# Optimization experiments

Hardware: AMD Instinct MI355X
Metric: run time of the kernel (lower is better)

Reference implementation:

```python
import jax, jax.numpy as jnp
import numpy as np

B, L, S, H = 2, 256, 384, 768
Tc, Dc = 16, 50
WV, WD = 20000, 100
CV = 128
NEG = -1e30


def _lstm_scan(x, Wih, Whh, bih, bhh):
    # x: [N, T, D] -> hs: [N, T, Hc]; torch LSTM gate order i,f,g,o
    N = x.shape[0]
    Hc = Whh.shape[1]
    h0 = jnp.zeros((N, Hc), x.dtype)

    def step(carry, xt):
        h, c = carry
        g = xt @ Wih.T + h @ Whh.T + bih + bhh  # [N, 4Hc]
        i, f, gg, o = jnp.split(g, 4, axis=-1)
        i = jax.nn.sigmoid(i)
        f = jax.nn.sigmoid(f)
        gg = jnp.tanh(gg)
        o = jax.nn.sigmoid(o)
        c = f * c + i * gg
        h = o * jnp.tanh(c)
        return (h, c), h

    _, hs = jax.lax.scan(step, (h0, h0), jnp.swapaxes(x, 0, 1))
    return jnp.swapaxes(hs, 0, 1)


def setup_inputs() -> dict:
    key = jax.random.key(0)
    ks = jax.random.split(key, 10)
    bert_emb = jax.random.normal(ks[0], (B, S, H), jnp.float32)
    pieces2word = jax.random.randint(ks[1], (B, L, S), 0, 2, jnp.int32)
    word_ids = jax.random.randint(ks[2], (B, L), 0, WV, jnp.int32)
    char_count = jax.random.randint(ks[3], (B, L), 1, Tc + 1, jnp.int32)
    char_ids = jax.random.randint(ks[4], (B, L, Tc), 0, CV, jnp.int32)
    # mask consistent with ragged char lengths (first char_count positions valid)
    token_masks_char = (jnp.arange(Tc)[None, None, :] < char_count[..., None]).astype(jnp.int32)
    word_table = jax.random.normal(ks[5], (WV, WD), jnp.float32) * 0.02
    char_table = jax.random.normal(ks[6], (CV, Dc), jnp.float32) * 0.02
    sc = 1.0 / np.sqrt(Dc)

    def lstm_w(k):
        a, b, c, d = jax.random.split(k, 4)
        return (jax.random.uniform(a, (4 * Dc, Dc), jnp.float32, -sc, sc),
                jax.random.uniform(b, (4 * Dc, Dc), jnp.float32, -sc, sc),
                jax.random.uniform(c, (4 * Dc,), jnp.float32, -sc, sc),
                jax.random.uniform(d, (4 * Dc,), jnp.float32, -sc, sc))

    Wih_f, Whh_f, bih_f, bhh_f = lstm_w(ks[7])
    Wih_b, Whh_b, bih_b, bhh_b = lstm_w(ks[8])
    return dict(bert_emb=bert_emb, pieces2word=pieces2word, word_ids=word_ids,
                char_count=char_count, char_ids=char_ids, token_masks_char=token_masks_char,
                word_table=word_table, char_table=char_table,
                Wih_f=Wih_f, Whh_f=Whh_f, bih_f=bih_f, bhh_f=bhh_f,
                Wih_b=Wih_b, Whh_b=Whh_b, bih_b=bih_b, bhh_b=bhh_b)


def reference(bert_emb, pieces2word, word_ids, char_count, char_ids, token_masks_char,
              word_table, char_table, Wih_f, Whh_f, bih_f, bhh_f, Wih_b, Whh_b, bih_b, bhh_b):
    # --- piece2word max pool (expand + masked_fill(min) + max over pieces) ---
    minv = jnp.min(bert_emb)
    # [B, L, S, H] intermediate, as in the original expand
    masked = jnp.where(pieces2word[..., None] != 0, bert_emb[:, None, :, :], minv)
    word_reps = jnp.max(masked, axis=2)  # [B, L, H]
    # dropouts are identity in eval mode

    # --- word embedding lookup ---
    word_embed = word_table[word_ids]  # [B, L, WD]

    # --- char bi-LSTM with packed-sequence semantics ---
    lens = jnp.maximum(char_count.reshape(-1), 1)  # char_count[char_count==0]=1
    x = char_table[char_ids.reshape(B * L, Tc)]  # [N, Tc, Dc]
    h_fwd = _lstm_scan(x, Wih_f, Whh_f, bih_f, bhh_f)
    # reverse each sequence within its valid length for the backward direction
    t = jnp.arange(Tc)[None, :]
    idx = jnp.where(t < lens[:, None], lens[:, None] - 1 - t, t)  # [N, Tc]
    x_rev = jnp.take_along_axis(x, idx[..., None], axis=1)
    h_bwd = _lstm_scan(x_rev, Wih_b, Whh_b, bih_b, bhh_b)
    h_bwd = jnp.take_along_axis(h_bwd, idx[..., None], axis=1)  # back to original order
    h = jnp.concatenate([h_fwd, h_bwd], axis=-1)  # [N, Tc, 2*Dc]
    valid = (t < lens[:, None])[..., None]
    h = jnp.where(valid, h, 0.0)  # pad_packed_sequence zero-pads beyond length
    h = h.reshape(B, L, Tc, 2 * Dc)

    # --- combine(..., 'max'): masked max over ragged char groups ---
    m = jnp.where(token_masks_char[..., None] == 0, NEG, 0.0)
    sup = jnp.max(m + h, axis=2)  # [B, L, 2*Dc]
    sup = jnp.where(sup == NEG, 0.0, sup)

    return jnp.concatenate([word_reps, word_embed, sup], axis=-1)  # [B, L, H+WD+2*Dc]
```

## Files before the change

### kernel.cpp

```cpp
#include <hip/hip_runtime.h>
#include <float.h>

#define Bb 2
#define Ll 256
#define Ss 384
#define Hh 768
#define Tc 16
#define Dc 50
#define WD 100
#define OUTC 968


__global__ void init_ws(unsigned* wmin) {
    if (blockIdx.x == 0 && threadIdx.x == 0) *wmin = 0xFFFFFFFFu;
}

__device__ inline unsigned enc_f32(float f) {
    unsigned k = __float_as_uint(f);
    return (k & 0x80000000u) ? ~k : (k | 0x80000000u);
}
__device__ inline float dec_f32(unsigned k) {
    unsigned bits = (k & 0x80000000u) ? (k ^ 0x80000000u) : ~k;
    return __uint_as_float(bits);
}

__global__ void min_reduce(const float* __restrict__ x, int n, unsigned* wmin) {
    int i = blockIdx.x * blockDim.x + threadIdx.x;
    float m = FLT_MAX;
    for (; i < n; i += gridDim.x * blockDim.x) m = fminf(m, x[i]);
    #pragma unroll
    for (int off = 32; off; off >>= 1) m = fminf(m, __shfl_down(m, off, 64));
    if ((threadIdx.x & 63) == 0) atomicMin(wmin, enc_f32(m));
}


#define NCHUNK 4
#define SCHUNK (Ss / NCHUNK)
#define LT 8

__global__ __launch_bounds__(256) void word_reps_partial(
        const float* __restrict__ bert, const int* __restrict__ p2w,
        float* __restrict__ partial) {
    int blk = blockIdx.x;
    int hc = blk % 3;
    int lt = (blk / 3) % 32;
    int bc = blk / (3 * 32);
    int b  = bc >> 2;
    int ch = bc & 3;
    int h  = hc * 256 + threadIdx.x;
    int l0 = lt * LT;

    float acc[LT];
    #pragma unroll
    for (int i = 0; i < LT; i++) acc[i] = -FLT_MAX;

    const float* bb = bert + ((size_t)b * Ss) * Hh + h;
    const int*   pm = p2w + ((size_t)b * Ll + l0) * Ss;
    int s0 = ch * SCHUNK;
    for (int s = s0; s < s0 + SCHUNK; s++) {
        float v = bb[(size_t)s * Hh];
        #pragma unroll
        for (int i = 0; i < LT; i++) {
            int m = pm[i * Ss + s];
            acc[i] = fmaxf(acc[i], m ? v : -FLT_MAX);
        }
    }
    #pragma unroll
    for (int i = 0; i < LT; i++)
        partial[(((size_t)ch * Bb + b) * Ll + (l0 + i)) * Hh + h] = acc[i];
}


__device__ inline float tanh_fast(float x) {
    float e = __expf(2.f * x);
    return 1.f - 2.f / (e + 1.f);
}
__device__ inline float sigmoid_fast(float x) {
    return 1.f / (1.f + __expf(-x));
}

__global__ __launch_bounds__(256) void lstm_kernel(
        const int* __restrict__ char_ids, const int* __restrict__ char_count,
        const float* __restrict__ char_table,
        const float* __restrict__ Wih_f, const float* __restrict__ Whh_f,
        const float* __restrict__ bih_f, const float* __restrict__ bhh_f,
        const float* __restrict__ Wih_b, const float* __restrict__ Whh_b,
        const float* __restrict__ bih_b, const float* __restrict__ bhh_b,
        float* __restrict__ out) {
    int n   = blockIdx.x;
    int dir = blockIdx.y;
    const float* Wih = dir ? Wih_b : Wih_f;
    const float* Whh = dir ? Whh_b : Whh_f;
    const float* bih = dir ? bih_b : bih_f;
    const float* bhh = dir ? bhh_b : bhh_f;
    int tid = threadIdx.x;

    __shared__ __align__(16) float xs[Tc][52];
    __shared__ float xp[Tc][200];
    __shared__ float gs[200];
    __shared__ __align__(16) float hs[52];

    int len = char_count[n];
    if (len < 1) len = 1;

    for (int e = tid; e < Tc * 52; e += 256) {
        int t = e / 52, d = e - t * 52;
        int st = dir ? (t < len ? len - 1 - t : t) : t;
        float v = 0.f;
        if (d < Dc) v = char_table[char_ids[n * Tc + st] * Dc + d];
        xs[t][d] = v;
    }
    if (tid < 52) hs[tid] = 0.f;
    __syncthreads();

    float w[52];
    float bias = 0.f;
    if (tid < 200) {
        #pragma unroll
        for (int j = 0; j < Dc; j++) w[j] = Wih[tid * Dc + j];
        w[50] = 0.f; w[51] = 0.f;
        bias = bih[tid] + bhh[tid];
        for (int t = 0; t < Tc; t++) {
            float a = bias;
            #pragma unroll
            for (int j = 0; j < 52; j += 4) {
                float4 xv = *(const float4*)&xs[t][j];
                a += xv.x * w[j] + xv.y * w[j+1] + xv.z * w[j+2] + xv.w * w[j+3];
            }
            xp[t][tid] = a;
        }
        #pragma unroll
        for (int j = 0; j < Dc; j++) w[j] = Whh[tid * Dc + j];
    }
    __syncthreads();

    float c = 0.f, maxv = -FLT_MAX;
    for (int t = 0; t < Tc; t++) {
        if (tid < 200) {
            float g = xp[t][tid];
            #pragma unroll
            for (int j = 0; j < 52; j += 4) {
                float4 hv = *(const float4*)&hs[j];
                g += hv.x * w[j] + hv.y * w[j+1] + hv.z * w[j+2] + hv.w * w[j+3];
            }
            gs[tid] = g;
        }
        __syncthreads();
        if (tid < Dc) {
            float si = sigmoid_fast(gs[tid]);
            float sf = sigmoid_fast(gs[tid + 50]);
            float tg = tanh_fast(gs[tid + 100]);
            float so = sigmoid_fast(gs[tid + 150]);
            c = sf * c + si * tg;
            float h = so * tanh_fast(c);
            hs[tid] = h;
            if (t < len) maxv = fmaxf(maxv, h);
        }
        __syncthreads();
    }
    if (tid < Dc)
        out[(size_t)n * OUTC + (Hh + WD) + dir * Dc + tid] = maxv;
}


__global__ __launch_bounds__(256) void finalize(
        const float* __restrict__ partial, const unsigned* __restrict__ wmin,
        const int* __restrict__ word_ids, const float* __restrict__ word_table,
        float* __restrict__ out) {
    int idx = blockIdx.x * blockDim.x + threadIdx.x;
    if (idx >= Bb * Ll * OUTC) return;
    int col = idx % OUTC;
    int bl  = idx / OUTC;
    if (col < Hh) {
        float m = -FLT_MAX;
        #pragma unroll
        for (int ch = 0; ch < NCHUNK; ch++)
            m = fmaxf(m, partial[((size_t)ch * Bb * Ll + bl) * Hh + col]);
        if (m == -FLT_MAX) m = dec_f32(*wmin);
        out[idx] = m;
    } else if (col < Hh + WD) {
        out[idx] = word_table[(size_t)word_ids[bl] * WD + (col - Hh)];
    }
}

extern "C" void kernel_launch(void* const* d_in, const int* in_sizes, int n_in,
                              void* d_out, int out_size, void* d_ws, size_t ws_size,
                              hipStream_t stream) {
    const float* bert       = (const float*)d_in[0];
    const int*   p2w        = (const int*)d_in[1];
    const int*   word_ids   = (const int*)d_in[2];
    const int*   char_count = (const int*)d_in[3];
    const int*   char_ids   = (const int*)d_in[4];
    const float* word_table = (const float*)d_in[6];
    const float* char_table = (const float*)d_in[7];
    const float* Wih_f = (const float*)d_in[8];
    const float* Whh_f = (const float*)d_in[9];
    const float* bih_f = (const float*)d_in[10];
    const float* bhh_f = (const float*)d_in[11];
    const float* Wih_b = (const float*)d_in[12];
    const float* Whh_b = (const float*)d_in[13];
    const float* bih_b = (const float*)d_in[14];
    const float* bhh_b = (const float*)d_in[15];
    float* out = (float*)d_out;

    unsigned* wmin  = (unsigned*)d_ws;
    float* partial  = (float*)((char*)d_ws + 256);

    init_ws<<<1, 64, 0, stream>>>(wmin);
    min_reduce<<<256, 256, 0, stream>>>(bert, Bb * Ss * Hh, wmin);
    word_reps_partial<<<768, 256, 0, stream>>>(bert, p2w, partial);
    lstm_kernel<<<dim3(512, 2), 256, 0, stream>>>(
        char_ids, char_count, char_table,
        Wih_f, Whh_f, bih_f, bhh_f, Wih_b, Whh_b, bih_b, bhh_b, out);
    finalize<<<(Bb * Ll * OUTC + 255) / 256, 256, 0, stream>>>(
        partial, wmin, word_ids, word_table, out);
}
```

Before: 153.9 us.

## Precompute char input projections, fuse prep work, and write word reps directly

The input-to-hidden LSTM projection is precomputed once per vocabulary character (128 chars x 2 directions) into a table, so the per-word LSTM blocks only gather their gate pre-activations. The min reduction, the projection table and the word-embedding gather are merged into a single prep kernel. The word max-pool now runs over the full sequence per block with 4 rows per block and writes straight to the output, which removes the partial buffer, the atomics and the finalize pass. The cost is fewer, longer-running word blocks and a dependency on the prep kernel.

```diff
diff --git a/kernel.cpp b/kernel.cpp
--- a/kernel.cpp
+++ b/kernel.cpp
@@ -8,67 +8,9 @@
 #define Tc 16
 #define Dc 50
 #define WD 100
+#define CV 128
+#define NG 200
 #define OUTC 968
-
-
-__global__ void init_ws(unsigned* wmin) {
-    if (blockIdx.x == 0 && threadIdx.x == 0) *wmin = 0xFFFFFFFFu;
-}
-
-__device__ inline unsigned enc_f32(float f) {
-    unsigned k = __float_as_uint(f);
-    return (k & 0x80000000u) ? ~k : (k | 0x80000000u);
-}
-__device__ inline float dec_f32(unsigned k) {
-    unsigned bits = (k & 0x80000000u) ? (k ^ 0x80000000u) : ~k;
-    return __uint_as_float(bits);
-}
-
-__global__ void min_reduce(const float* __restrict__ x, int n, unsigned* wmin) {
-    int i = blockIdx.x * blockDim.x + threadIdx.x;
-    float m = FLT_MAX;
-    for (; i < n; i += gridDim.x * blockDim.x) m = fminf(m, x[i]);
-    #pragma unroll
-    for (int off = 32; off; off >>= 1) m = fminf(m, __shfl_down(m, off, 64));
-    if ((threadIdx.x & 63) == 0) atomicMin(wmin, enc_f32(m));
-}
-
-
-#define NCHUNK 4
-#define SCHUNK (Ss / NCHUNK)
-#define LT 8
-
-__global__ __launch_bounds__(256) void word_reps_partial(
-        const float* __restrict__ bert, const int* __restrict__ p2w,
-        float* __restrict__ partial) {
-    int blk = blockIdx.x;
-    int hc = blk % 3;
-    int lt = (blk / 3) % 32;
-    int bc = blk / (3 * 32);
-    int b  = bc >> 2;
-    int ch = bc & 3;
-    int h  = hc * 256 + threadIdx.x;
-    int l0 = lt * LT;
-
-    float acc[LT];
-    #pragma unroll
-    for (int i = 0; i < LT; i++) acc[i] = -FLT_MAX;
-
-    const float* bb = bert + ((size_t)b * Ss) * Hh + h;
-    const int*   pm = p2w + ((size_t)b * Ll + l0) * Ss;
-    int s0 = ch * SCHUNK;
-    for (int s = s0; s < s0 + SCHUNK; s++) {
-        float v = bb[(size_t)s * Hh];
-        #pragma unroll
-        for (int i = 0; i < LT; i++) {
-            int m = pm[i * Ss + s];
-            acc[i] = fmaxf(acc[i], m ? v : -FLT_MAX);
-        }
-    }
-    #pragma unroll
-    for (int i = 0; i < LT; i++)
-        partial[(((size_t)ch * Bb + b) * Ll + (l0 + i)) * Hh + h] = acc[i];
-}
 
 
 __device__ inline float tanh_fast(float x) {
@@ -79,65 +21,129 @@
     return 1.f / (1.f + __expf(-x));
 }
 
+
+__global__ __launch_bounds__(256) void prep_kernel(
+        const float* __restrict__ bert, const float* __restrict__ char_table,
+        const float* __restrict__ Wih_f, const float* __restrict__ bih_f, const float* __restrict__ bhh_f,
+        const float* __restrict__ Wih_b, const float* __restrict__ bih_b, const float* __restrict__ bhh_b,
+        const int* __restrict__ word_ids, const float* __restrict__ word_table,
+        float* __restrict__ minp, float* __restrict__ xpt, float* __restrict__ out) {
+    int blk = blockIdx.x, tid = threadIdx.x;
+    if (blk < 256) {
+        const int n = Bb * Ss * Hh;
+        float m = FLT_MAX;
+        for (int i = blk * 256 + tid; i < n; i += 256 * 256) m = fminf(m, bert[i]);
+        #pragma unroll
+        for (int off = 32; off; off >>= 1) m = fminf(m, __shfl_down(m, off, 64));
+        __shared__ float red[4];
+        if ((tid & 63) == 0) red[tid >> 6] = m;
+        __syncthreads();
+        if (tid == 0) minp[blk] = fminf(fminf(red[0], red[1]), fminf(red[2], red[3]));
+    } else if (blk < 512) {
+        int idx = blk - 256;
+        int dir = idx >> 7, cid = idx & 127;
+        const float* Wih = dir ? Wih_b : Wih_f;
+        const float* bih = dir ? bih_b : bih_f;
+        const float* bhh = dir ? bhh_b : bhh_f;
+        __shared__ float ct[Dc];
+        if (tid < Dc) ct[tid] = char_table[cid * Dc + tid];
+        __syncthreads();
+        if (tid < NG) {
+            float a = bih[tid] + bhh[tid];
+            #pragma unroll
+            for (int j = 0; j < Dc; j++) a += Wih[tid * Dc + j] * ct[j];
+            xpt[idx * NG + tid] = a;
+        }
+    } else {
+        for (int i = (blk - 512) * 256 + tid; i < Bb * Ll * WD; i += 64 * 256) {
+            int bl = i / WD, d = i - bl * WD;
+            out[(size_t)bl * OUTC + Hh + d] = word_table[(size_t)word_ids[bl] * WD + d];
+        }
+    }
+}
+
+
+__global__ __launch_bounds__(256) void word_kernel(
+        const float* __restrict__ bert, const int* __restrict__ p2w,
+        const float* __restrict__ minp, float* __restrict__ out) {
+    int tid = threadIdx.x;
+    __shared__ float sminv;
+    if (tid < 64) {
+        float m = fminf(fminf(minp[tid], minp[tid + 64]),
+                        fminf(minp[tid + 128], minp[tid + 192]));
+        #pragma unroll
+        for (int off = 32; off; off >>= 1) m = fminf(m, __shfl_down(m, off, 64));
+        if (tid == 0) sminv = m;
+    }
+    __syncthreads();
+    int blk = blockIdx.x;
+    int hc = blk % 3;
+    int lt = (blk / 3) & 63;
+    int b  = blk / 192;
+    int h  = hc * 256 + tid;
+    int l0 = lt * 4;
+
+    float acc[4];
+    #pragma unroll
+    for (int i = 0; i < 4; i++) acc[i] = -FLT_MAX;
+
+    const float* bb = bert + (size_t)b * Ss * Hh + h;
+    const int*   pm = p2w + ((size_t)b * Ll + l0) * Ss;
+    for (int s = 0; s < Ss; s++) {
+        float v = bb[(size_t)s * Hh];
+        #pragma unroll
+        for (int i = 0; i < 4; i++) {
+            int m = pm[i * Ss + s];
+            acc[i] = fmaxf(acc[i], m ? v : -FLT_MAX);
+        }
+    }
+    float mv = sminv;
+    #pragma unroll
+    for (int i = 0; i < 4; i++) {
+        float a = (acc[i] == -FLT_MAX) ? mv : acc[i];
+        out[((size_t)(b * Ll + l0 + i)) * OUTC + h] = a;
+    }
+}
+
+
 __global__ __launch_bounds__(256) void lstm_kernel(
         const int* __restrict__ char_ids, const int* __restrict__ char_count,
-        const float* __restrict__ char_table,
-        const float* __restrict__ Wih_f, const float* __restrict__ Whh_f,
-        const float* __restrict__ bih_f, const float* __restrict__ bhh_f,
-        const float* __restrict__ Wih_b, const float* __restrict__ Whh_b,
-        const float* __restrict__ bih_b, const float* __restrict__ bhh_b,
-        float* __restrict__ out) {
-    int n   = blockIdx.x;
-    int dir = blockIdx.y;
-    const float* Wih = dir ? Wih_b : Wih_f;
+        const float* __restrict__ Whh_f, const float* __restrict__ Whh_b,
+        const float* __restrict__ xpt, float* __restrict__ out) {
+    int n = blockIdx.x, dir = blockIdx.y, tid = threadIdx.x;
     const float* Whh = dir ? Whh_b : Whh_f;
-    const float* bih = dir ? bih_b : bih_f;
-    const float* bhh = dir ? bhh_b : bhh_f;
-    int tid = threadIdx.x;
-
-    __shared__ __align__(16) float xs[Tc][52];
-    __shared__ float xp[Tc][200];
-    __shared__ float gs[200];
+
+    __shared__ float xg[Tc][NG];
+    __shared__ float gs[NG];
     __shared__ __align__(16) float hs[52];
+    __shared__ int scid[Tc];
 
     int len = char_count[n];
     if (len < 1) len = 1;
-
-    for (int e = tid; e < Tc * 52; e += 256) {
-        int t = e / 52, d = e - t * 52;
+    if (tid < Tc) {
+        int t = tid;
         int st = dir ? (t < len ? len - 1 - t : t) : t;
-        float v = 0.f;
-        if (d < Dc) v = char_table[char_ids[n * Tc + st] * Dc + d];
-        xs[t][d] = v;
+        scid[t] = char_ids[n * Tc + st];
     }
     if (tid < 52) hs[tid] = 0.f;
     __syncthreads();
 
+    for (int e = tid; e < Tc * NG; e += 256) {
+        int t = e / NG, g = e - t * NG;
+        xg[t][g] = xpt[(dir * CV + scid[t]) * NG + g];
+    }
     float w[52];
-    float bias = 0.f;
-    if (tid < 200) {
-        #pragma unroll
-        for (int j = 0; j < Dc; j++) w[j] = Wih[tid * Dc + j];
+    if (tid < NG) {
+        #pragma unroll
+        for (int j = 0; j < Dc; j++) w[j] = Whh[tid * Dc + j];
         w[50] = 0.f; w[51] = 0.f;
-        bias = bih[tid] + bhh[tid];
-        for (int t = 0; t < Tc; t++) {
-            float a = bias;
-            #pragma unroll
-            for (int j = 0; j < 52; j += 4) {
-                float4 xv = *(const float4*)&xs[t][j];
-                a += xv.x * w[j] + xv.y * w[j+1] + xv.z * w[j+2] + xv.w * w[j+3];
-            }
-            xp[t][tid] = a;
-        }
-        #pragma unroll
-        for (int j = 0; j < Dc; j++) w[j] = Whh[tid * Dc + j];
     }
     __syncthreads();
 
     float c = 0.f, maxv = -FLT_MAX;
     for (int t = 0; t < Tc; t++) {
-        if (tid < 200) {
-            float g = xp[t][tid];
+        if (tid < NG) {
+            float g = xg[t][tid];
             #pragma unroll
             for (int j = 0; j < 52; j += 4) {
                 float4 hv = *(const float4*)&hs[j];
@@ -160,27 +166,6 @@
     }
     if (tid < Dc)
         out[(size_t)n * OUTC + (Hh + WD) + dir * Dc + tid] = maxv;
-}
-
-
-__global__ __launch_bounds__(256) void finalize(
-        const float* __restrict__ partial, const unsigned* __restrict__ wmin,
-        const int* __restrict__ word_ids, const float* __restrict__ word_table,
-        float* __restrict__ out) {
-    int idx = blockIdx.x * blockDim.x + threadIdx.x;
-    if (idx >= Bb * Ll * OUTC) return;
-    int col = idx % OUTC;
-    int bl  = idx / OUTC;
-    if (col < Hh) {
-        float m = -FLT_MAX;
-        #pragma unroll
-        for (int ch = 0; ch < NCHUNK; ch++)
-            m = fmaxf(m, partial[((size_t)ch * Bb * Ll + bl) * Hh + col]);
-        if (m == -FLT_MAX) m = dec_f32(*wmin);
-        out[idx] = m;
-    } else if (col < Hh + WD) {
-        out[idx] = word_table[(size_t)word_ids[bl] * WD + (col - Hh)];
-    }
 }
 
 extern "C" void kernel_launch(void* const* d_in, const int* in_sizes, int n_in,
@@ -203,15 +188,13 @@
     const float* bhh_b = (const float*)d_in[15];
     float* out = (float*)d_out;
 
-    unsigned* wmin  = (unsigned*)d_ws;
-    float* partial  = (float*)((char*)d_ws + 256);
-
-    init_ws<<<1, 64, 0, stream>>>(wmin);
-    min_reduce<<<256, 256, 0, stream>>>(bert, Bb * Ss * Hh, wmin);
-    word_reps_partial<<<768, 256, 0, stream>>>(bert, p2w, partial);
+    float* minp = (float*)d_ws;
+    float* xpt  = minp + 256;
+
+    prep_kernel<<<576, 256, 0, stream>>>(
+        bert, char_table, Wih_f, bih_f, bhh_f, Wih_b, bih_b, bhh_b,
+        word_ids, word_table, minp, xpt, out);
+    word_kernel<<<384, 256, 0, stream>>>(bert, p2w, minp, out);
     lstm_kernel<<<dim3(512, 2), 256, 0, stream>>>(
-        char_ids, char_count, char_table,
-        Wih_f, Whh_f, bih_f, bhh_f, Wih_b, Whh_b, bih_b, bhh_b, out);
-    finalize<<<(Bb * Ll * OUTC + 255) / 256, 256, 0, stream>>>(
-        partial, wmin, word_ids, word_table, out);
-}
+        char_ids, char_count, Whh_f, Whh_b, xpt, out);
+}
```

After: 151.4 us. Within noise of the previous version (-1.7%).
